# Kernel tuning notes

Measured on AMD Instinct MI355X. Metric: run time of the kernel, lower is better.

## Reference

```python
import math
import jax, jax.numpy as jnp
import numpy as np

D_MODEL, STATE_DIM, SEQ_L = 256, 64, 8192


def setup_inputs() -> dict:
    key = jax.random.key(0)
    ks = jax.random.split(key, 6)
    d, N = D_MODEL, STATE_DIM
    s = 1.0 / math.sqrt(N)
    return {
        "Lambda_re": jax.random.normal(ks[0], (d, N), jnp.float32),
        "Lambda_im": jax.random.normal(ks[1], (d, N), jnp.float32),
        "P_re": jax.random.normal(ks[2], (d, N), jnp.float32) * s,
        "P_im": jax.random.normal(ks[3], (d, N), jnp.float32) * s,
        "B_re": jax.random.normal(ks[4], (d, N), jnp.float32) * s,
        "B_im": jnp.zeros((d, N), jnp.float32),
        "log_dt": jax.random.uniform(ks[5], (d,), jnp.float32,
                                     math.log(1e-3), math.log(0.1)),
        "D": jnp.zeros((d,), jnpp := jnp.float32) if False else jnp.zeros((d,), jnp.float32),
        "L": SEQ_L,
    }


def reference(Lambda_re, Lambda_im, P_re, P_im, B_re, B_im, log_dt, D, L):
    # NPLR / Cauchy-Woodbury S4 kernel (learn_cd=False -> C = B, D is a zero buffer)
    Lam = (-jax.nn.softplus(Lambda_re) + 1j * Lambda_im).astype(jnp.complex64)  # [d, N]
    P = (P_re + 1j * P_im).astype(jnp.complex64)                                # [d, N]
    B = (B_re + 1j * B_im).astype(jnp.complex64)                                # [d, N]
    dt = jnp.exp(log_dt)                                                        # [d]

    k = jnp.arange(L)
    z = jnp.exp((-2j * jnp.pi / L) * k).astype(jnp.complex64)                   # [L] roots of unity
    eps = jnp.finfo(jnp.float32).eps
    denom_z = 1.0 + z
    denom_z = jnp.where(jnp.abs(denom_z) < eps, jnp.complex64(eps), denom_z)

    # Bilinear-transform frequencies g: [d, L] complex
    g = (2.0 / dt)[:, None] * ((1.0 - z) / denom_z)[None, :]

    # Cauchy resolvent R: [d, L, N] complex (the dominant intermediate)
    R = 1.0 / (g[:, :, None] - Lam[:, None, :])

    Pc, Bc = jnp.conj(P), jnp.conj(B)
    PRB = jnp.einsum('dn,dln,dn->dl', Pc, R, B)
    PRP = jnp.einsum('dn,dln,dn->dl', Pc, R, P)
    BRB = jnp.einsum('dn,dln,dn->dl', Bc, R, B)
    BRP = jnp.einsum('dn,dln,dn->dl', Bc, R, P)

    # Woodbury rank-1 correction, then undo the bilinear prefactor
    K_hat = (2.0 / denom_z)[None, :] * (BRB - BRP * PRB / (1.0 + PRP))          # [d, L]
    K = jnp.fft.ifft(K_hat, n=L, axis=-1).real.astype(jnp.float32)
    return (K, D)
```

## Files before the change

### kernel.cpp

```cpp
#include <hip/hip_runtime.h>
#include <math.h>

#ifndef M_PI
#define M_PI 3.14159265358979323846
#endif

#define DMODEL 256
#define NSTATE 64
#define LSEQ   8192
#define INVL   (1.0f/8192.0f)

typedef float v2f __attribute__((ext_vector_type(2)));

#define OFF_TW  0
#define OFF_DN  (6144*8)
#define OFF_CDT (OFF_DN + DMODEL*NSTATE*48)
#define OFF_KT  (OFF_CDT + 1024)

__device__ __forceinline__ float sin_rev(float r) {
#if __has_builtin(__builtin_amdgcn_sinf)
  return __builtin_amdgcn_sinf(r);
#else
  return __sinf(r * 6.283185307179586f);
#endif
}
__device__ __forceinline__ float cos_rev(float r) {
#if __has_builtin(__builtin_amdgcn_cosf)
  return __builtin_amdgcn_cosf(r);
#else
  return __cosf(r * 6.283185307179586f);
#endif
}

__device__ __forceinline__ float2 cmul(float2 a, float2 b) {
  return make_float2(a.x*b.x - a.y*b.y, a.x*b.y + a.y*b.x);
}

__device__ __forceinline__ float2 woodbury(float2 S1, float2 S2, float2 S3,
                                           float2 S4, float T) {
  float nr = (S1.x*S1.x - S1.y*S1.y) + (S2.x*S2.x - S2.y*S2.y);
  float ni = 2.0f*(S1.x*S1.y + S2.x*S2.y);
  float dr = 1.0f + S3.x, di = S3.y;
  float inv = __builtin_amdgcn_rcpf(fmaf(dr, dr, di*di));
  float qr = (nr*dr + ni*di) * inv;
  float qi = (ni*dr - nr*di) * inv;
  float vr = S4.x - qr, vi = S4.y - qi;
  return make_float2((vr - T*vi)*INVL, (vi + T*vr)*INVL);
}

__global__ __launch_bounds__(256) void precompute_kernel(
    const float* __restrict__ Lre, const float* __restrict__ Lim,
    const float* __restrict__ Pre, const float* __restrict__ Pim,
    const float* __restrict__ Bre, const float* __restrict__ Bim,
    const float* __restrict__ log_dt, char* __restrict__ ws)
{
  const int t = blockIdx.x * blockDim.x + threadIdx.x;
  float2* tw  = (float2*)(ws + OFF_TW);
  float4* dn  = (float4*)(ws + OFF_DN);
  float*  cdt = (float*)(ws + OFF_CDT);

  if (t < 6144) {
    double th = (2.0 * M_PI / (double)LSEQ) * (double)t;
    double s, c; sincos(th, &s, &c);
    tw[t] = make_float2((float)c, (float)s);
  }
  {
    float lre = Lre[t], lim = Lim[t];
    float pre = Pre[t], pim = Pim[t];
    float bre = Bre[t], bim = Bim[t];
    float sp = fmaxf(lre, 0.0f) + log1pf(expf(-fabsf(lre)));
    float w1r = pre*bre + pim*bim;
    float w1i = pre*bim - pim*bre;
    float w2  = pre*pre + pim*pim;
    float w3  = bre*bre + bim*bim;
    dn[3*t]   = make_float4(lim, sp*sp, w1r*sp, w1i*sp);
    dn[3*t+1] = make_float4(w2*sp, w3*sp, w1r, w1i);
    dn[3*t+2] = make_float4(w2, w3, 0.0f, 0.0f);
  }
  if (t < DMODEL) cdt[t] = 2.0f * expf(-log_dt[t]);
}

__global__ __launch_bounds__(256, 8) void cauchy_kernel(
    const float4* __restrict__ dn_all, const float* __restrict__ cdt,
    float4* __restrict__ kt)
{
  const int d = blockIdx.y;
  const int b = blockIdx.x * 256 + threadIdx.x;
  const float4* dn = dn_all + (size_t)d * (3*NSTATE);
  const float c = cdt[d];

  const unsigned r = __brev((unsigned)(2*b)) >> 19;
  const int kA = (int)(((r & 0x0555u) << 1) | ((r & 0x0AAAu) >> 1));
  const float rev = (float)kA * (1.0f/16384.0f);
  const float sA = sin_rev(rev), cA = cos_rev(rev);
  float TA =  sA * __builtin_amdgcn_rcpf(cA);
  float TB = -cA * __builtin_amdgcn_rcpf(sA);
  TA = fminf(fmaxf(TA, -1e7f), 1e7f);
  TB = fminf(fmaxf(TB, -1e7f), 1e7f);
  const v2f g2 = {c * TA, c * TB};

  v2f S1x = {0,0}, S1y = {0,0}, S2x = {0,0}, S2y = {0,0};
  v2f S3x = {0,0}, S3y = {0,0}, S4x = {0,0}, S4y = {0,0};

#pragma unroll 4
  for (int n = 0; n < NSTATE; ++n) {
    const float4 q0 = dn[3*n];
    const float4 q1 = dn[3*n+1];
    const float4 q2 = dn[3*n+2];
    const v2f dim = g2 - q0.x;
    const v2f mag = __builtin_elementwise_fma(dim, dim, (v2f)(q0.y));
    const float p = mag.x * mag.y;
    const float rp = __builtin_amdgcn_rcpf(p);
    const v2f inv = rp * (v2f){mag.y, mag.x};
    const v2f dI  = dim * inv;
    S1x = __builtin_elementwise_fma((v2f)(q0.z), inv, S1x);
    S1y = __builtin_elementwise_fma((v2f)(q1.z), -dI, S1y);
    S2x = __builtin_elementwise_fma((v2f)(q0.w), inv, S2x);
    S2y = __builtin_elementwise_fma((v2f)(q1.w), -dI, S2y);
    S3x = __builtin_elementwise_fma((v2f)(q1.x), inv, S3x);
    S3y = __builtin_elementwise_fma((v2f)(q2.x), -dI, S3y);
    S4x = __builtin_elementwise_fma((v2f)(q1.y), inv, S4x);
    S4y = __builtin_elementwise_fma((v2f)(q2.y), -dI, S4y);
  }
  const float2 KA = woodbury(make_float2(S1x.x, S1y.x), make_float2(S2x.x, S2y.x),
                             make_float2(S3x.x, S3y.x), make_float2(S4x.x, S4y.x), TA);
  const float2 KB = woodbury(make_float2(S1x.y, S1y.y), make_float2(S2x.y, S2y.y),
                             make_float2(S3x.y, S3y.y), make_float2(S4x.y, S4y.y), TB);
  kt[(size_t)d * 4096 + b] = make_float4(KA.x + KB.x, KA.y + KB.y,
                                         KA.x - KB.x, KA.y - KB.y);
}

__global__ __launch_bounds__(1024) void ifft_kernel(
    const float4* __restrict__ kt, const float2* __restrict__ tw,
    const float* __restrict__ Din, float* __restrict__ out)
{
  __shared__ __align__(16) float2 xy[LSEQ];
  const int d = blockIdx.x;
  const int t = threadIdx.x;
  const float4* row = kt + (size_t)d * 4096;

  for (int i = t; i < 4096; i += 1024) ((float4*)xy)[i] = row[i];
  __syncthreads();

#pragma unroll
  for (int s = 0; s < 6; ++s) {
    const int h = 2 << (2*s);
    const int twsh = 10 - 2*s;
#pragma unroll
    for (int j = 0; j < 2; ++j) {
      const int bb = t + (j << 10);
      const int pos = bb & (h - 1);
      const int i0 = ((bb >> (1 + 2*s)) << (3 + 2*s)) + pos;
      const int ti = pos << twsh;
      const float2 w1 = tw[ti];
      const float2 w2 = tw[2*ti];
      const float2 w3 = tw[3*ti];
      const float2 x0 = xy[i0];
      const float2 x1 = xy[i0 + h];
      const float2 x2 = xy[i0 + 2*h];
      const float2 x3 = xy[i0 + 3*h];
      const float2 t1 = cmul(w1, x1);
      const float2 t2 = cmul(w2, x2);
      const float2 t3 = cmul(w3, x3);
      const float2 u0 = make_float2(x0.x + t2.x, x0.y + t2.y);
      const float2 u1 = make_float2(x0.x - t2.x, x0.y - t2.y);
      const float2 u2 = make_float2(t1.x + t3.x, t1.y + t3.y);
      const float2 vv = make_float2(t1.x - t3.x, t1.y - t3.y);
      xy[i0]         = make_float2(u0.x + u2.x, u0.y + u2.y);
      xy[i0 + h]     = make_float2(u1.x - vv.y, u1.y + vv.x);
      xy[i0 + 2*h]   = make_float2(u0.x - u2.x, u0.y - u2.y);
      xy[i0 + 3*h]   = make_float2(u1.x + vv.y, u1.y - vv.x);
    }
    __syncthreads();
  }

  float* orow = out + (size_t)d * LSEQ;
  for (int i = t; i < LSEQ; i += 1024) orow[i] = xy[i].x;

  if (d == 0 && t < DMODEL) out[(size_t)DMODEL * LSEQ + t] = Din[t];
}

extern "C" void kernel_launch(void* const* d_in, const int* in_sizes, int n_in,
                              void* d_out, int out_size, void* d_ws, size_t ws_size,
                              hipStream_t stream)
{
  const float* Lre    = (const float*)d_in[0];
  const float* Lim    = (const float*)d_in[1];
  const float* Pre    = (const float*)d_in[2];
  const float* Pim    = (const float*)d_in[3];
  const float* Bre    = (const float*)d_in[4];
  const float* Bim    = (const float*)d_in[5];
  const float* log_dt = (const float*)d_in[6];
  const float* Din    = (const float*)d_in[7];
  float* out = (float*)d_out;
  char* ws = (char*)d_ws;

  hipLaunchKernelGGL(precompute_kernel, dim3(64), dim3(256), 0, stream,
                     Lre, Lim, Pre, Pim, Bre, Bim, log_dt, ws);
  hipLaunchKernelGGL(cauchy_kernel, dim3(16, DMODEL), dim3(256), 0, stream,
                     (const float4*)(ws + OFF_DN), (const float*)(ws + OFF_CDT),
                     (float4*)(ws + OFF_KT));
  hipLaunchKernelGGL(ifft_kernel, dim3(DMODEL), dim3(1024), 0, stream,
                     (const float4*)(ws + OFF_KT), (const float2*)(ws + OFF_TW),
                     Din, out);
}
```

Measured before the change: 126.1 us.

## Compact Cauchy coefficients, use per-lane reciprocals, fuse last FFT stage with output store

The per-state coefficient table shrinks from three float4 to two by factoring the softplus term out of the weights and multiplying it into the reciprocal once per state. The shared reciprocal trick (one rcp of the product) is replaced by two independent reciprocals, which saves multiplies but costs an extra transcendental. The final radix-4 IFFT stage now writes only the real parts straight to global memory, skipping its shared-memory store, the trailing barrier and the separate copy-out loop. The Cauchy kernel is compute-bound, so the net effect depends on whether rcp throughput outweighs the saved FMAs and loads.

```diff
diff --git a/kernel.cpp b/kernel.cpp
--- a/kernel.cpp
+++ b/kernel.cpp
@@ -14,7 +14,7 @@
 
 #define OFF_TW  0
 #define OFF_DN  (6144*8)
-#define OFF_CDT (OFF_DN + DMODEL*NSTATE*48)
+#define OFF_CDT (OFF_DN + DMODEL*NSTATE*32)
 #define OFF_KT  (OFF_CDT + 1024)
 
 __device__ __forceinline__ float sin_rev(float r) {
@@ -73,9 +73,8 @@
     float w1i = pre*bim - pim*bre;
     float w2  = pre*pre + pim*pim;
     float w3  = bre*bre + bim*bim;
-    dn[3*t]   = make_float4(lim, sp*sp, w1r*sp, w1i*sp);
-    dn[3*t+1] = make_float4(w2*sp, w3*sp, w1r, w1i);
-    dn[3*t+2] = make_float4(w2, w3, 0.0f, 0.0f);
+    dn[2*t]   = make_float4(lim, sp*sp, sp, 0.0f);
+    dn[2*t+1] = make_float4(w1r, w1i, w2, w3);
   }
   if (t < DMODEL) cdt[t] = 2.0f * expf(-log_dt[t]);
 }
@@ -86,7 +85,7 @@
 {
   const int d = blockIdx.y;
   const int b = blockIdx.x * 256 + threadIdx.x;
-  const float4* dn = dn_all + (size_t)d * (3*NSTATE);
+  const float4* dn = dn_all + (size_t)d * (2*NSTATE);
   const float c = cdt[d];
 
   const unsigned r = __brev((unsigned)(2*b)) >> 19;
@@ -104,23 +103,22 @@
 
 #pragma unroll 4
   for (int n = 0; n < NSTATE; ++n) {
-    const float4 q0 = dn[3*n];
-    const float4 q1 = dn[3*n+1];
-    const float4 q2 = dn[3*n+2];
+    const float4 q0 = dn[2*n];
+    const float4 qw = dn[2*n+1];
     const v2f dim = g2 - q0.x;
     const v2f mag = __builtin_elementwise_fma(dim, dim, (v2f)(q0.y));
-    const float p = mag.x * mag.y;
-    const float rp = __builtin_amdgcn_rcpf(p);
-    const v2f inv = rp * (v2f){mag.y, mag.x};
-    const v2f dI  = dim * inv;
-    S1x = __builtin_elementwise_fma((v2f)(q0.z), inv, S1x);
-    S1y = __builtin_elementwise_fma((v2f)(q1.z), -dI, S1y);
-    S2x = __builtin_elementwise_fma((v2f)(q0.w), inv, S2x);
-    S2y = __builtin_elementwise_fma((v2f)(q1.w), -dI, S2y);
-    S3x = __builtin_elementwise_fma((v2f)(q1.x), inv, S3x);
-    S3y = __builtin_elementwise_fma((v2f)(q2.x), -dI, S3y);
-    S4x = __builtin_elementwise_fma((v2f)(q1.y), inv, S4x);
-    S4y = __builtin_elementwise_fma((v2f)(q2.y), -dI, S4y);
+    const v2f inv = {__builtin_amdgcn_rcpf(mag.x),
+                     __builtin_amdgcn_rcpf(mag.y)};
+    const v2f spinv = q0.z * inv;
+    const v2f dI    = dim * inv;
+    S1x = __builtin_elementwise_fma((v2f)(qw.x), spinv, S1x);
+    S1y = __builtin_elementwise_fma((v2f)(qw.x), -dI, S1y);
+    S2x = __builtin_elementwise_fma((v2f)(qw.y), spinv, S2x);
+    S2y = __builtin_elementwise_fma((v2f)(qw.y), -dI, S2y);
+    S3x = __builtin_elementwise_fma((v2f)(qw.z), spinv, S3x);
+    S3y = __builtin_elementwise_fma((v2f)(qw.z), -dI, S3y);
+    S4x = __builtin_elementwise_fma((v2f)(qw.w), spinv, S4x);
+    S4y = __builtin_elementwise_fma((v2f)(qw.w), -dI, S4y);
   }
   const float2 KA = woodbury(make_float2(S1x.x, S1y.x), make_float2(S2x.x, S2y.x),
                              make_float2(S3x.x, S3y.x), make_float2(S4x.x, S4y.x), TA);
@@ -138,12 +136,13 @@
   const int d = blockIdx.x;
   const int t = threadIdx.x;
   const float4* row = kt + (size_t)d * 4096;
+  float* orow = out + (size_t)d * LSEQ;
 
   for (int i = t; i < 4096; i += 1024) ((float4*)xy)[i] = row[i];
   __syncthreads();
 
 #pragma unroll
-  for (int s = 0; s < 6; ++s) {
+  for (int s = 0; s < 5; ++s) {
     const int h = 2 << (2*s);
     const int twsh = 10 - 2*s;
 #pragma unroll
@@ -174,8 +173,27 @@
     __syncthreads();
   }
 
-  float* orow = out + (size_t)d * LSEQ;
-  for (int i = t; i < LSEQ; i += 1024) orow[i] = xy[i].x;
+#pragma unroll
+  for (int j = 0; j < 2; ++j) {
+    const int bb = t + (j << 10);
+    const float2 w1 = tw[bb];
+    const float2 w2 = tw[2*bb];
+    const float2 w3 = tw[3*bb];
+    const float2 x0 = xy[bb];
+    const float2 x1 = xy[bb + 2048];
+    const float2 x2 = xy[bb + 4096];
+    const float2 x3 = xy[bb + 6144];
+    const float2 t1 = cmul(w1, x1);
+    const float2 t2 = cmul(w2, x2);
+    const float2 t3 = cmul(w3, x3);
+    const float u0r = x0.x + t2.x, u1r = x0.x - t2.x;
+    const float u2r = t1.x + t3.x;
+    const float vvi = t1.y - t3.y;
+    orow[bb]        = u0r + u2r;
+    orow[bb + 2048] = u1r - vvi;
+    orow[bb + 4096] = u0r - u2r;
+    orow[bb + 6144] = u1r + vvi;
+  }
 
   if (d == 0 && t < DMODEL) out[(size_t)DMODEL * LSEQ + t] = Din[t];
 }
```

New measurement: 125.6 us. No clear change (-0.4%).
